# Optimization experiments

Hardware: AMD Instinct MI355X
Metric: run time of the kernel (lower is better)

The kernel has to match this reference:

```python
import jax, jax.numpy as jnp
import numpy as np

HEADS = 12
D_HEAD = 64  # d_model // heads


def _split_heads(t, heads, d_head):
    # Faithful to the torch code: transpose(1,2) -> (B, C, T), then
    # reshape (B, -1, heads, d_head), then transpose(1,2) -> (B, heads, T', d_head).
    B = t.shape[0]
    t = jnp.swapaxes(t, 1, 2)                      # (B, C, T)
    t = t.reshape(B, -1, heads, d_head)            # (B, T', heads, d_head) -- layout quirk preserved
    return jnp.swapaxes(t, 1, 2)                   # (B, heads, T', d_head)


def setup_inputs() -> dict:
    key = jax.random.key(0)
    ks = jax.random.split(key, 10)
    B, Tq, Tkv, D = 8, 4096, 77, 768
    s = 0.02
    return {
        "x": jax.random.normal(ks[0], (B, Tq, D), jnp.float32),
        "prompt": jax.random.normal(ks[1], (B, Tkv, D), jnp.float32),
        "Wq": jax.random.normal(ks[2], (D, D), jnp.float32) * s,
        "bq": jax.random.normal(ks[3], (D,), jnp.float32) * s,
        "Wk": jax.random.normal(ks[4], (D, D), jnp.float32) * s,
        "bk": jax.random.normal(ks[5], (D,), jnp.float32) * s,
        "Wv": jax.random.normal(ks[6], (D, D), jnp.float32) * s,
        "bv": jax.random.normal(ks[7], (D,), jnp.float32) * s,
        "Wp": jax.random.normal(ks[8], (D, D), jnp.float32) * s,
        "bp": jax.random.normal(ks[9], (D,), jnp.float32) * s,
    }


def reference(x, prompt, Wq, bq, Wk, bk, Wv, bv, Wp, bp):
    B, Tq, C = x.shape
    Ckv = prompt.shape[-1]
    q = _split_heads(x @ Wq.T + bq, HEADS, D_HEAD)       # (B, H, Tq, d_head)
    k = _split_heads(prompt @ Wk.T + bk, HEADS, D_HEAD)  # (B, H, Tkv, d_head)
    v = _split_heads(prompt @ Wv.T + bv, HEADS, D_HEAD)
    scale = 1.0 / jnp.sqrt(jnp.asarray(Ckv, x.dtype))    # note: sqrt(d_prompt), as in source
    att = jnp.einsum('bhqd,bhkd->bhqk', q, k) * scale
    att = jax.nn.softmax(att, axis=-1)
    out = jnp.einsum('bhqk,bhkd->bhqd', att, v)          # (B, H, Tq, d_head)
    out = jnp.swapaxes(out, 1, 2).reshape(B, Tq, C)
    return out @ Wp.T + bp                               # dropout = identity (eval)
```

## Files before the change

### kernel.cpp

```cpp
#include <hip/hip_runtime.h>

typedef __attribute__((ext_vector_type(8))) __bf16 bf16x8;
typedef __attribute__((ext_vector_type(4))) float f32x4;
typedef __attribute__((ext_vector_type(8))) unsigned short u16x8;
typedef __attribute__((ext_vector_type(4))) unsigned short u16x4;

#define DEV __device__ __forceinline__

DEV float bf2f(unsigned short u) {
  unsigned int x = ((unsigned int)u) << 16;
  return __builtin_bit_cast(float, x);
}
DEV unsigned short f2bf(float f) {
  unsigned int u = __builtin_bit_cast(unsigned int, f);
  u = u + 0x7fffu + ((u >> 16) & 1u);
  return (unsigned short)(u >> 16);
}

DEV void glds16(const void* g, void* l) {
  __builtin_amdgcn_global_load_lds(
      (__attribute__((address_space(1))) void*)g,
      (__attribute__((address_space(3))) void*)l, 16, 0, 0);
}

__global__ __launch_bounds__(256) void k_prep(
    const float* __restrict__ x, const float* __restrict__ Wq,
    const float* __restrict__ Wk, const float* __restrict__ Wv,
    const float* __restrict__ Wp, const float* __restrict__ prompt,
    const float* __restrict__ bk, const float* __restrict__ bv,
    unsigned short* __restrict__ xb, unsigned short* __restrict__ wqb,
    unsigned short* __restrict__ wkvb, unsigned short* __restrict__ wpb,
    unsigned short* __restrict__ pb, float* __restrict__ bkv,
    unsigned short* __restrict__ vt2) {
  const int blk = blockIdx.x;
  const int tid = threadIdx.x;
  if (blk < 2048) {
    for (int i = blk * 256 + tid; i < 6291456; i += 524288) {
      float4 v = reinterpret_cast<const float4*>(x)[i];
      u16x4 o;
      o[0] = f2bf(v.x); o[1] = f2bf(v.y); o[2] = f2bf(v.z); o[3] = f2bf(v.w);
      reinterpret_cast<u16x4*>(xb)[i] = o;
    }
  } else if (blk < 4352) {
    const int w = (blk - 2048) / 576;
    const int i = (blk - 2048 - w * 576) * 256 + tid;
    const float* src = (w == 0) ? Wq : (w == 1) ? Wk : (w == 2) ? Wv : Wp;
    unsigned short* dst =
        (w == 0) ? wqb : (w == 1) ? wkvb : (w == 2) ? (wkvb + 589824) : wpb;
    float4 v = reinterpret_cast<const float4*>(src)[i];
    u16x4 o;
    o[0] = f2bf(v.x); o[1] = f2bf(v.y); o[2] = f2bf(v.z); o[3] = f2bf(v.w);
    reinterpret_cast<u16x4*>(dst)[i] = o;
  } else if (blk < 5120) {
    const int i4 = (blk - 4352) * 256 + tid;
    const int e = i4 * 4;
    const int b = e / 98304;
    const int rem = e - b * 98304;
    const int s = rem / 768;
    const int d = rem - s * 768;
    u16x4 o;
    if (s < 77) {
      float4 v = *reinterpret_cast<const float4*>(&prompt[((long)b * 77 + s) * 768 + d]);
      o[0] = f2bf(v.x); o[1] = f2bf(v.y); o[2] = f2bf(v.z); o[3] = f2bf(v.w);
    } else {
      o[0] = 0; o[1] = 0; o[2] = 0; o[3] = 0;
    }
    reinterpret_cast<u16x4*>(pb)[i4] = o;
  } else if (blk < 5126) {
    const int i = (blk - 5120) * 256 + tid;
    if (i < 1536) bkv[i] = (i < 768) ? bk[i] : bv[i - 768];
  } else {
    const int i = (blk - 5126) * 256 + tid;
    u16x8 z = {};
    reinterpret_cast<u16x8*>(vt2)[i] = z;
  }
}

__global__ __launch_bounds__(256, 2) void k_gemmkv(const unsigned short* __restrict__ A,
                                                   const unsigned short* __restrict__ B, long sB,
                                                   unsigned short* __restrict__ Kv,
                                                   unsigned short* __restrict__ Vt2,
                                                   const float* __restrict__ bias) {
  __shared__ alignas(16) unsigned short As[128 * 64];
  __shared__ alignas(16) unsigned short Bs[128 * 64];

  const int bz = blockIdx.z;
  const unsigned short* Bb = B + (long)bz * sB;

  const int tid = threadIdx.x;
  const int wave = tid >> 6;
  const int lane = tid & 63;
  const int tm = blockIdx.y * 128;
  const int wm = (wave >> 1) * 64;
  const int wn = (wave & 1) * 64;
  const int fr = lane & 15;
  const int fk = (lane >> 4) * 8;
  const int srow = lane >> 3;
  const int scol = (lane & 7) * 8;

  f32x4 acc[4][4] = {};

  for (int k0 = 0; k0 < 768; k0 += 64) {
    __syncthreads();
#pragma unroll
    for (int i = 0; i < 4; ++i) {
      const int chunk = i * 4 + wave;
      glds16(A + (long)(tm + chunk * 8 + srow) * 768 + (k0 + scol), &As[chunk * 512]);
    }
#pragma unroll
    for (int i = 0; i < 4; ++i) {
      const int chunk = i * 4 + wave;
      glds16(Bb + (long)(chunk * 8 + srow) * 768 + (k0 + scol), &Bs[chunk * 512]);
    }
    __syncthreads();
#pragma unroll
    for (int ks = 0; ks < 2; ++ks) {
      bf16x8 af[4], bf[4];
#pragma unroll
      for (int mi = 0; mi < 4; ++mi)
        af[mi] = *reinterpret_cast<const bf16x8*>(&As[(wm + mi * 16 + fr) * 64 + ks * 32 + fk]);
#pragma unroll
      for (int ni = 0; ni < 4; ++ni)
        bf[ni] = *reinterpret_cast<const bf16x8*>(&Bs[(wn + ni * 16 + fr) * 64 + ks * 32 + fk]);
#pragma unroll
      for (int mi = 0; mi < 4; ++mi)
#pragma unroll
        for (int ni = 0; ni < 4; ++ni)
          acc[mi][ni] =
              __builtin_amdgcn_mfma_f32_16x16x32_bf16(af[mi], bf[ni], acc[mi][ni], 0, 0, 0);
    }
  }

  const int r0 = (lane >> 4) * 4;
#pragma unroll
  for (int mi = 0; mi < 4; ++mi) {
#pragma unroll
    for (int ni = 0; ni < 4; ++ni) {
      const int col = wn + ni * 16 + fr;
      if (col < 77) {
#pragma unroll
        for (int r = 0; r < 4; ++r) {
          const int row = tm + wm + mi * 16 + r0 + r;
          const unsigned short v = f2bf(acc[mi][ni][r] + bias[row]);
          if (tm < 768) {
            Kv[(long)bz * 59136 + (long)row * 77 + col] = v;
          } else {
            const int p = (row - 768) * 77 + col;
            const int snew = p / 768;
            const int c0 = p - snew * 768;
            Vt2[(long)bz * 79872 + (long)c0 * 104 + snew] = v;
          }
        }
      }
    }
  }
}

template <int QUIRK>
__global__ __launch_bounds__(256, 2) void k_g128(const unsigned short* __restrict__ A,
                                                 const unsigned short* __restrict__ B,
                                                 void* __restrict__ Cv,
                                                 const float* __restrict__ bias) {
  __shared__ alignas(16) unsigned short S[17408];
  unsigned short* const As = S;
  unsigned short* const Bs = S + 8192;

  const int tid = threadIdx.x;
  const int wave = tid >> 6;
  const int lane = tid & 63;
  const int l = (blockIdx.x & 7) * 192 + (blockIdx.x >> 3);
  const int tm = (QUIRK ? (l % 6) : (l / 6)) * 128;
  const int tn = (QUIRK ? (l / 6) : (l % 6)) * 128;
  const int wm = (wave >> 1) * 64;
  const int wn = (wave & 1) * 64;
  const int fr = lane & 15;
  const int fk = (lane >> 4) * 8;
  const int srow = lane >> 3;
  const int srcx = ((lane & 7) ^ srow) * 8;
  const int rx = (fr & 7) * 8;

  f32x4 acc[4][4] = {};

  for (int k0 = 0; k0 < 768; k0 += 64) {
    __syncthreads();
#pragma unroll
    for (int i = 0; i < 4; ++i) {
      const int chunk = i * 4 + wave;
      glds16(A + (long)(tm + chunk * 8 + srow) * 768 + (k0 + srcx), &As[chunk * 512]);
    }
#pragma unroll
    for (int i = 0; i < 4; ++i) {
      const int chunk = i * 4 + wave;
      glds16(B + (long)(tn + chunk * 8 + srow) * 768 + (k0 + srcx), &Bs[chunk * 512]);
    }
    __syncthreads();
#pragma unroll
    for (int ks = 0; ks < 2; ++ks) {
      bf16x8 af[4], bf[4];
#pragma unroll
      for (int mi = 0; mi < 4; ++mi)
        af[mi] = *reinterpret_cast<const bf16x8*>(
            &As[(wm + mi * 16 + fr) * 64 + ((ks * 32 + fk) ^ rx)]);
#pragma unroll
      for (int ni = 0; ni < 4; ++ni)
        bf[ni] = *reinterpret_cast<const bf16x8*>(
            &Bs[(wn + ni * 16 + fr) * 64 + ((ks * 32 + fk) ^ rx)]);
#pragma unroll
      for (int mi = 0; mi < 4; ++mi)
#pragma unroll
        for (int ni = 0; ni < 4; ++ni)
          acc[mi][ni] =
              __builtin_amdgcn_mfma_f32_16x16x32_bf16(af[mi], bf[ni], acc[mi][ni], 0, 0, 0);
    }
  }

  const int r0 = (lane >> 4) * 4;

  if (QUIRK) {
    __syncthreads();
#pragma unroll
    for (int mi = 0; mi < 4; ++mi)
#pragma unroll
      for (int ni = 0; ni < 4; ++ni)
#pragma unroll
        for (int r = 0; r < 4; ++r) {
          const int cm = wm + mi * 16 + r0 + r;
          const int ct = wn + ni * 16 + fr;
          S[cm * 136 + ct] = f2bf(acc[mi][ni][r] + bias[tm + cm]);
        }
    __syncthreads();
    unsigned short* qt = (unsigned short*)Cv;
    const int b_ = tn >> 12;
    const int toff = tn & 4095;
    const int cm = tid >> 1;
    const int t8 = (tid & 1) * 64;
    const long gb = (long)b_ * 3145728 + (long)(tm + cm) * 4096 + toff + t8;
#pragma unroll
    for (int j = 0; j < 8; ++j)
      *reinterpret_cast<u16x8*>(&qt[gb + j * 8]) =
          *reinterpret_cast<const u16x8*>(&S[cm * 136 + t8 + j * 8]);
  } else {
    float* out = (float*)Cv;
#pragma unroll
    for (int mi = 0; mi < 4; ++mi) {
#pragma unroll
      for (int ni = 0; ni < 4; ++ni) {
        const int col = tn + wn + ni * 16 + fr;
        const float bv = bias[col];
#pragma unroll
        for (int r = 0; r < 4; ++r) {
          const long g = tm + wm + mi * 16 + r0 + r;
          out[g * 768 + col] = acc[mi][ni][r] + bv;
        }
      }
    }
  }
}

__global__ __launch_bounds__(256, 4) void k_attn(const unsigned short* __restrict__ QT,
                                                 const unsigned short* __restrict__ KVT,
                                                 const unsigned short* __restrict__ VT2,
                                                 unsigned short* __restrict__ Y) {
  __shared__ alignas(16) unsigned short Plds[128 * 104];
  __shared__ alignas(16) unsigned short Vt[64 * 104];

  const int b = blockIdx.z;
  const int h = blockIdx.y;
  const int tid = threadIdx.x;
  const int wave = tid >> 6;
  const int lane = tid & 63;
  const int fr = lane & 15;
  const int fg = lane >> 4;

  const unsigned short* vsrc = VT2 + (long)b * 79872 + h * 6656;
#pragma unroll
  for (int r = 0; r < 4; ++r) {
    const int chunk = r * 256 + tid;
    if (chunk < 832) glds16(vsrc + chunk * 8, &Vt[chunk * 8]);
  }

  {
    const int row = wave * 32 + (lane >> 1);
    u16x8 z = {};
    *reinterpret_cast<u16x8*>(&Plds[row * 104 + 80 + (lane & 1) * 8]) = z;
  }

  const int t0 = blockIdx.x * 128 + wave * 32;
  const long qb = (long)b * 3145728 + h * 64;
  const long kflat = (long)b * 59136 + h * 64;

  bf16x8 qa[2][2];
#pragma unroll
  for (int m = 0; m < 2; ++m)
#pragma unroll
    for (int ks = 0; ks < 2; ++ks)
      qa[m][ks] = *reinterpret_cast<const bf16x8*>(
          &QT[qb + (long)(t0 + m * 16 + fr) * 768 + ks * 32 + fg * 8]);

  bf16x8 kb[5][2];
#pragma unroll
  for (int n = 0; n < 5; ++n)
#pragma unroll
    for (int ks = 0; ks < 2; ++ks)
      kb[n][ks] = *reinterpret_cast<const bf16x8*>(
          &KVT[kflat + (long)(n * 16 + fr) * 768 + ks * 32 + fg * 8]);

  f32x4 s_[2][5] = {};
#pragma unroll
  for (int ks = 0; ks < 2; ++ks)
#pragma unroll
    for (int m = 0; m < 2; ++m)
#pragma unroll
      for (int n = 0; n < 5; ++n)
        s_[m][n] = __builtin_amdgcn_mfma_f32_16x16x32_bf16(qa[m][ks], kb[n][ks], s_[m][n], 0, 0, 0);

  const float scale = 0.036084391824351615f;
  f32x4 rl[2];
#pragma unroll
  for (int m = 0; m < 2; ++m) {
#pragma unroll
    for (int n = 0; n < 5; ++n) {
      const int key = n * 16 + fr;
#pragma unroll
      for (int r = 0; r < 4; ++r)
        s_[m][n][r] = (key < 77) ? __expf(s_[m][n][r] * scale) : 0.f;
    }
    f32x4 t = s_[m][0] + s_[m][1] + s_[m][2] + s_[m][3] + s_[m][4];
#pragma unroll
    for (int w = 1; w < 16; w <<= 1) {
      f32x4 u;
#pragma unroll
      for (int r = 0; r < 4; ++r) u[r] = __shfl_xor(t[r], w);
      t += u;
    }
    rl[m][0] = 1.f / t[0]; rl[m][1] = 1.f / t[1];
    rl[m][2] = 1.f / t[2]; rl[m][3] = 1.f / t[3];
  }

#pragma unroll
  for (int m = 0; m < 2; ++m)
#pragma unroll
    for (int n = 0; n < 5; ++n)
#pragma unroll
      for (int r = 0; r < 4; ++r)
        Plds[(wave * 32 + m * 16 + fg * 4 + r) * 104 + n * 16 + fr] = f2bf(s_[m][n][r]);

  __syncthreads();

  f32x4 o[2][4] = {};
#pragma unroll
  for (int ks = 0; ks < 3; ++ks) {
    bf16x8 pa[2], vb[4];
#pragma unroll
    for (int m = 0; m < 2; ++m)
      pa[m] = *reinterpret_cast<const bf16x8*>(
          &Plds[(wave * 32 + m * 16 + fr) * 104 + ks * 32 + fg * 8]);
#pragma unroll
    for (int n = 0; n < 4; ++n)
      vb[n] = *reinterpret_cast<const bf16x8*>(&Vt[(n * 16 + fr) * 104 + ks * 32 + fg * 8]);
#pragma unroll
    for (int m = 0; m < 2; ++m)
#pragma unroll
      for (int n = 0; n < 4; ++n)
        o[m][n] = __builtin_amdgcn_mfma_f32_16x16x32_bf16(pa[m], vb[n], o[m][n], 0, 0, 0);
  }

#pragma unroll
  for (int m = 0; m < 2; ++m)
#pragma unroll
    for (int n = 0; n < 4; ++n)
#pragma unroll
      for (int r = 0; r < 4; ++r) {
        const int t = t0 + m * 16 + fg * 4 + r;
        const int d = n * 16 + fr;
        Y[qb + (long)t * 768 + d] = f2bf(o[m][n][r] * rl[m][r]);
      }
}

extern "C" void kernel_launch(void* const* d_in, const int* in_sizes, int n_in,
                              void* d_out, int out_size, void* d_ws, size_t ws_size,
                              hipStream_t stream) {
  const float* x      = (const float*)d_in[0];
  const float* prompt = (const float*)d_in[1];
  const float* Wq     = (const float*)d_in[2];
  const float* bq     = (const float*)d_in[3];
  const float* Wk     = (const float*)d_in[4];
  const float* bk     = (const float*)d_in[5];
  const float* Wv     = (const float*)d_in[6];
  const float* bv     = (const float*)d_in[7];
  const float* Wp     = (const float*)d_in[8];
  const float* bp     = (const float*)d_in[9];
  float* out = (float*)d_out;

  if (ws_size < 109185024u) return;
  char* ws = (char*)d_ws;
  unsigned short* xb   = (unsigned short*)(ws + 0);
  unsigned short* y    = xb;
  unsigned short* qt   = (unsigned short*)(ws + 50331648L);
  unsigned short* wqb  = (unsigned short*)(ws + 100663296L);
  unsigned short* wpb  = (unsigned short*)(ws + 101842944L);
  unsigned short* wkvb = (unsigned short*)(ws + 103022592L);
  unsigned short* pb   = (unsigned short*)(ws + 105381888L);
  unsigned short* kvt  = (unsigned short*)(ws + 106954752L);
  unsigned short* vt2  = (unsigned short*)(ws + 107900928L);
  float*          bkv  = (float*)(ws + 109178880L);

  k_prep<<<5438, 256, 0, stream>>>(x, Wq, Wk, Wv, Wp, prompt, bk, bv,
                                   xb, wqb, wkvb, wpb, pb, bkv, vt2);

  k_gemmkv<<<dim3(1, 12, 8), 256, 0, stream>>>(wkvb, pb, 98304L, kvt, vt2, bkv);

  k_g128<1><<<1536, 256, 0, stream>>>(wqb, xb, qt, bq);

  k_attn<<<dim3(32, 12, 8), 256, 0, stream>>>(qt, kvt, vt2, y);

  k_g128<0><<<1536, 256, 0, stream>>>(y, wpb, out, bp);
}
```

Measured before the change: 193.0 us.

## Merge KV and Q projection launches; pack bf16 converts and stage attention output

Folds the small K/V projection GEMM into the Q projection kernel as 96 extra blocks, removing one launch and letting the tiny KV work overlap with the Q GEMM. Replaces the scalar bf16 rounding with the packed v_cvt_pk_bf16_f32 instruction in the epilogues. The attention output is now staged through LDS and written as 16-byte vector stores instead of scattered 2-byte stores. The merged kernel adds a branch and uneven block costs, and the packed convert may round slightly differently from the manual routine.

```diff
diff --git a/kernel.cpp b/kernel.cpp
--- a/kernel.cpp
+++ b/kernel.cpp
@@ -15,6 +15,11 @@
   unsigned int u = __builtin_bit_cast(unsigned int, f);
   u = u + 0x7fffu + ((u >> 16) & 1u);
   return (unsigned short)(u >> 16);
+}
+DEV unsigned int cvtpk(float a, float b) {
+  unsigned int r;
+  asm("v_cvt_pk_bf16_f32 %0, %1, %2" : "=v"(r) : "v"(a), "v"(b));
+  return r;
 }
 
 DEV void glds16(const void* g, void* l) {
@@ -76,41 +81,107 @@
   }
 }
 
-__global__ __launch_bounds__(256, 2) void k_gemmkv(const unsigned short* __restrict__ A,
-                                                   const unsigned short* __restrict__ B, long sB,
-                                                   unsigned short* __restrict__ Kv,
-                                                   unsigned short* __restrict__ Vt2,
-                                                   const float* __restrict__ bias) {
-  __shared__ alignas(16) unsigned short As[128 * 64];
-  __shared__ alignas(16) unsigned short Bs[128 * 64];
-
-  const int bz = blockIdx.z;
-  const unsigned short* Bb = B + (long)bz * sB;
+__global__ __launch_bounds__(256, 2) void k_qkv(
+    const unsigned short* __restrict__ WQ, const unsigned short* __restrict__ XB,
+    unsigned short* __restrict__ QT, const float* __restrict__ BQ,
+    const unsigned short* __restrict__ WKV, const unsigned short* __restrict__ PB,
+    unsigned short* __restrict__ KV, unsigned short* __restrict__ VT2,
+    const float* __restrict__ BKV) {
+  __shared__ alignas(16) unsigned short S[17408];
+  unsigned short* const As = S;
+  unsigned short* const Bs = S + 8192;
 
   const int tid = threadIdx.x;
   const int wave = tid >> 6;
   const int lane = tid & 63;
-  const int tm = blockIdx.y * 128;
   const int wm = (wave >> 1) * 64;
   const int wn = (wave & 1) * 64;
   const int fr = lane & 15;
   const int fk = (lane >> 4) * 8;
   const int srow = lane >> 3;
-  const int scol = (lane & 7) * 8;
+  const int r0 = (lane >> 4) * 4;
+
+  if (blockIdx.x >= 1536) {
+    const int idx = blockIdx.x - 1536;
+    const int bz = idx / 12;
+    const int tm = (idx - bz * 12) * 128;
+    const unsigned short* Bb = PB + (long)bz * 98304;
+    const int scol = (lane & 7) * 8;
+
+    f32x4 acc[4][4] = {};
+    for (int k0 = 0; k0 < 768; k0 += 64) {
+      __syncthreads();
+#pragma unroll
+      for (int i = 0; i < 4; ++i) {
+        const int chunk = i * 4 + wave;
+        glds16(WKV + (long)(tm + chunk * 8 + srow) * 768 + (k0 + scol), &As[chunk * 512]);
+      }
+#pragma unroll
+      for (int i = 0; i < 4; ++i) {
+        const int chunk = i * 4 + wave;
+        glds16(Bb + (long)(chunk * 8 + srow) * 768 + (k0 + scol), &Bs[chunk * 512]);
+      }
+      __syncthreads();
+#pragma unroll
+      for (int ks = 0; ks < 2; ++ks) {
+        bf16x8 af[4], bf[4];
+#pragma unroll
+        for (int mi = 0; mi < 4; ++mi)
+          af[mi] = *reinterpret_cast<const bf16x8*>(&As[(wm + mi * 16 + fr) * 64 + ks * 32 + fk]);
+#pragma unroll
+        for (int ni = 0; ni < 4; ++ni)
+          bf[ni] = *reinterpret_cast<const bf16x8*>(&Bs[(wn + ni * 16 + fr) * 64 + ks * 32 + fk]);
+#pragma unroll
+        for (int mi = 0; mi < 4; ++mi)
+#pragma unroll
+          for (int ni = 0; ni < 4; ++ni)
+            acc[mi][ni] =
+                __builtin_amdgcn_mfma_f32_16x16x32_bf16(af[mi], bf[ni], acc[mi][ni], 0, 0, 0);
+      }
+    }
+#pragma unroll
+    for (int mi = 0; mi < 4; ++mi) {
+#pragma unroll
+      for (int ni = 0; ni < 4; ++ni) {
+        const int col = wn + ni * 16 + fr;
+        if (col < 77) {
+#pragma unroll
+          for (int r = 0; r < 4; ++r) {
+            const int row = tm + wm + mi * 16 + r0 + r;
+            const unsigned short v = f2bf(acc[mi][ni][r] + BKV[row]);
+            if (tm < 768) {
+              KV[(long)bz * 59136 + (long)row * 77 + col] = v;
+            } else {
+              const int p = (row - 768) * 77 + col;
+              const int snew = p / 768;
+              const int c0 = p - snew * 768;
+              VT2[(long)bz * 79872 + (long)c0 * 104 + snew] = v;
+            }
+          }
+        }
+      }
+    }
+    return;
+  }
+
+  const int l = (blockIdx.x & 7) * 192 + (blockIdx.x >> 3);
+  const int tm = (l % 6) * 128;
+  const int tn = (l / 6) * 128;
+  const int srcx = ((lane & 7) ^ srow) * 8;
+  const int rx = (fr & 7) * 8;
 
   f32x4 acc[4][4] = {};
-
   for (int k0 = 0; k0 < 768; k0 += 64) {
     __syncthreads();
 #pragma unroll
     for (int i = 0; i < 4; ++i) {
       const int chunk = i * 4 + wave;
-      glds16(A + (long)(tm + chunk * 8 + srow) * 768 + (k0 + scol), &As[chunk * 512]);
+      glds16(WQ + (long)(tm + chunk * 8 + srow) * 768 + (k0 + srcx), &As[chunk * 512]);
     }
 #pragma unroll
     for (int i = 0; i < 4; ++i) {
       const int chunk = i * 4 + wave;
-      glds16(Bb + (long)(chunk * 8 + srow) * 768 + (k0 + scol), &Bs[chunk * 512]);
+      glds16(XB + (long)(tn + chunk * 8 + srow) * 768 + (k0 + srcx), &Bs[chunk * 512]);
     }
     __syncthreads();
 #pragma unroll
@@ -118,10 +189,12 @@
       bf16x8 af[4], bf[4];
 #pragma unroll
       for (int mi = 0; mi < 4; ++mi)
-        af[mi] = *reinterpret_cast<const bf16x8*>(&As[(wm + mi * 16 + fr) * 64 + ks * 32 + fk]);
+        af[mi] = *reinterpret_cast<const bf16x8*>(
+            &As[(wm + mi * 16 + fr) * 64 + ((ks * 32 + fk) ^ rx)]);
 #pragma unroll
       for (int ni = 0; ni < 4; ++ni)
-        bf[ni] = *reinterpret_cast<const bf16x8*>(&Bs[(wn + ni * 16 + fr) * 64 + ks * 32 + fk]);
+        bf[ni] = *reinterpret_cast<const bf16x8*>(
+            &Bs[(wn + ni * 16 + fr) * 64 + ((ks * 32 + fk) ^ rx)]);
 #pragma unroll
       for (int mi = 0; mi < 4; ++mi)
 #pragma unroll
@@ -131,37 +204,40 @@
     }
   }
 
-  const int r0 = (lane >> 4) * 4;
+  __syncthreads();
 #pragma unroll
   for (int mi = 0; mi < 4; ++mi) {
+    const int cmb = wm + mi * 16 + r0;
 #pragma unroll
     for (int ni = 0; ni < 4; ++ni) {
-      const int col = wn + ni * 16 + fr;
-      if (col < 77) {
-#pragma unroll
-        for (int r = 0; r < 4; ++r) {
-          const int row = tm + wm + mi * 16 + r0 + r;
-          const unsigned short v = f2bf(acc[mi][ni][r] + bias[row]);
-          if (tm < 768) {
-            Kv[(long)bz * 59136 + (long)row * 77 + col] = v;
-          } else {
-            const int p = (row - 768) * 77 + col;
-            const int snew = p / 768;
-            const int c0 = p - snew * 768;
-            Vt2[(long)bz * 79872 + (long)c0 * 104 + snew] = v;
-          }
-        }
-      }
-    }
-  }
-}
-
-template <int QUIRK>
-__global__ __launch_bounds__(256, 2) void k_g128(const unsigned short* __restrict__ A,
+      const int ct = wn + ni * 16 + fr;
+      const unsigned int p01 =
+          cvtpk(acc[mi][ni][0] + BQ[tm + cmb], acc[mi][ni][1] + BQ[tm + cmb + 1]);
+      const unsigned int p23 =
+          cvtpk(acc[mi][ni][2] + BQ[tm + cmb + 2], acc[mi][ni][3] + BQ[tm + cmb + 3]);
+      S[(cmb + 0) * 136 + ct] = (unsigned short)p01;
+      S[(cmb + 1) * 136 + ct] = (unsigned short)(p01 >> 16);
+      S[(cmb + 2) * 136 + ct] = (unsigned short)p23;
+      S[(cmb + 3) * 136 + ct] = (unsigned short)(p23 >> 16);
+    }
+  }
+  __syncthreads();
+  const int b_ = tn >> 12;
+  const int toff = tn & 4095;
+  const int cm = tid >> 1;
+  const int t8 = (tid & 1) * 64;
+  const long gb = (long)b_ * 3145728 + (long)(tm + cm) * 4096 + toff + t8;
+#pragma unroll
+  for (int j = 0; j < 8; ++j)
+    *reinterpret_cast<u16x8*>(&QT[gb + j * 8]) =
+        *reinterpret_cast<const u16x8*>(&S[cm * 136 + t8 + j * 8]);
+}
+
+__global__ __launch_bounds__(256, 2) void k_gout(const unsigned short* __restrict__ A,
                                                  const unsigned short* __restrict__ B,
-                                                 void* __restrict__ Cv,
+                                                 float* __restrict__ out,
                                                  const float* __restrict__ bias) {
-  __shared__ alignas(16) unsigned short S[17408];
+  __shared__ alignas(16) unsigned short S[16384];
   unsigned short* const As = S;
   unsigned short* const Bs = S + 8192;
 
@@ -169,8 +245,8 @@
   const int wave = tid >> 6;
   const int lane = tid & 63;
   const int l = (blockIdx.x & 7) * 192 + (blockIdx.x >> 3);
-  const int tm = (QUIRK ? (l % 6) : (l / 6)) * 128;
-  const int tn = (QUIRK ? (l / 6) : (l % 6)) * 128;
+  const int tm = (l / 6) * 128;
+  const int tn = (l % 6) * 128;
   const int wm = (wave >> 1) * 64;
   const int wn = (wave & 1) * 64;
   const int fr = lane & 15;
@@ -215,43 +291,16 @@
   }
 
   const int r0 = (lane >> 4) * 4;
-
-  if (QUIRK) {
-    __syncthreads();
-#pragma unroll
-    for (int mi = 0; mi < 4; ++mi)
-#pragma unroll
-      for (int ni = 0; ni < 4; ++ni)
-#pragma unroll
-        for (int r = 0; r < 4; ++r) {
-          const int cm = wm + mi * 16 + r0 + r;
-          const int ct = wn + ni * 16 + fr;
-          S[cm * 136 + ct] = f2bf(acc[mi][ni][r] + bias[tm + cm]);
-        }
-    __syncthreads();
-    unsigned short* qt = (unsigned short*)Cv;
-    const int b_ = tn >> 12;
-    const int toff = tn & 4095;
-    const int cm = tid >> 1;
-    const int t8 = (tid & 1) * 64;
-    const long gb = (long)b_ * 3145728 + (long)(tm + cm) * 4096 + toff + t8;
-#pragma unroll
-    for (int j = 0; j < 8; ++j)
-      *reinterpret_cast<u16x8*>(&qt[gb + j * 8]) =
-          *reinterpret_cast<const u16x8*>(&S[cm * 136 + t8 + j * 8]);
-  } else {
-    float* out = (float*)Cv;
-#pragma unroll
-    for (int mi = 0; mi < 4; ++mi) {
-#pragma unroll
-      for (int ni = 0; ni < 4; ++ni) {
-        const int col = tn + wn + ni * 16 + fr;
-        const float bv = bias[col];
-#pragma unroll
-        for (int r = 0; r < 4; ++r) {
-          const long g = tm + wm + mi * 16 + r0 + r;
-          out[g * 768 + col] = acc[mi][ni][r] + bv;
-        }
+#pragma unroll
+  for (int mi = 0; mi < 4; ++mi) {
+#pragma unroll
+    for (int ni = 0; ni < 4; ++ni) {
+      const int col = tn + wn + ni * 16 + fr;
+      const float bv = bias[col];
+#pragma unroll
+      for (int r = 0; r < 4; ++r) {
+        const long g = tm + wm + mi * 16 + r0 + r;
+        out[g * 768 + col] = acc[mi][ni][r] + bv;
       }
     }
   }
@@ -340,10 +389,16 @@
 #pragma unroll
   for (int m = 0; m < 2; ++m)
 #pragma unroll
-    for (int n = 0; n < 5; ++n)
-#pragma unroll
-      for (int r = 0; r < 4; ++r)
-        Plds[(wave * 32 + m * 16 + fg * 4 + r) * 104 + n * 16 + fr] = f2bf(s_[m][n][r]);
+    for (int n = 0; n < 5; ++n) {
+      const unsigned int p01 = cvtpk(s_[m][n][0], s_[m][n][1]);
+      const unsigned int p23 = cvtpk(s_[m][n][2], s_[m][n][3]);
+      const int base = wave * 32 + m * 16 + fg * 4;
+      const int col = n * 16 + fr;
+      Plds[(base + 0) * 104 + col] = (unsigned short)p01;
+      Plds[(base + 1) * 104 + col] = (unsigned short)(p01 >> 16);
+      Plds[(base + 2) * 104 + col] = (unsigned short)p23;
+      Plds[(base + 3) * 104 + col] = (unsigned short)(p23 >> 16);
+    }
 
   __syncthreads();
 
@@ -368,13 +423,24 @@
 #pragma unroll
   for (int m = 0; m < 2; ++m)
 #pragma unroll
-    for (int n = 0; n < 4; ++n)
-#pragma unroll
-      for (int r = 0; r < 4; ++r) {
-        const int t = t0 + m * 16 + fg * 4 + r;
-        const int d = n * 16 + fr;
-        Y[qb + (long)t * 768 + d] = f2bf(o[m][n][r] * rl[m][r]);
-      }
+    for (int n = 0; n < 4; ++n) {
+      const unsigned int p01 = cvtpk(o[m][n][0] * rl[m][0], o[m][n][1] * rl[m][1]);
+      const unsigned int p23 = cvtpk(o[m][n][2] * rl[m][2], o[m][n][3] * rl[m][3]);
+      const int base = wave * 32 + m * 16 + fg * 4;
+      const int col = n * 16 + fr;
+      Plds[(base + 0) * 104 + col] = (unsigned short)p01;
+      Plds[(base + 1) * 104 + col] = (unsigned short)(p01 >> 16);
+      Plds[(base + 2) * 104 + col] = (unsigned short)p23;
+      Plds[(base + 3) * 104 + col] = (unsigned short)(p23 >> 16);
+    }
+#pragma unroll
+  for (int j = 0; j < 4; ++j) {
+    const int chunk = j * 64 + lane;
+    const int row = chunk >> 3;
+    const int d8 = (chunk & 7) * 8;
+    *reinterpret_cast<u16x8*>(&Y[qb + (long)(t0 + row) * 768 + d8]) =
+        *reinterpret_cast<const u16x8*>(&Plds[(wave * 32 + row) * 104 + d8]);
+  }
 }
 
 extern "C" void kernel_launch(void* const* d_in, const int* in_sizes, int n_in,
@@ -408,11 +474,9 @@
   k_prep<<<5438, 256, 0, stream>>>(x, Wq, Wk, Wv, Wp, prompt, bk, bv,
                                    xb, wqb, wkvb, wpb, pb, bkv, vt2);
 
-  k_gemmkv<<<dim3(1, 12, 8), 256, 0, stream>>>(wkvb, pb, 98304L, kvt, vt2, bkv);
-
-  k_g128<1><<<1536, 256, 0, stream>>>(wqb, xb, qt, bq);
+  k_qkv<<<1632, 256, 0, stream>>>(wqb, xb, qt, bq, wkvb, pb, kvt, vt2, bkv);
 
   k_attn<<<dim3(32, 12, 8), 256, 0, stream>>>(qt, kvt, vt2, y);
 
-  k_g128<0><<<1536, 256, 0, stream>>>(y, wpb, out, bp);
-}
+  k_gout<<<1536, 256, 0, stream>>>(y, wpb, out, bp);
+}
```

New measurement: 181.7 us. -5.9%, faster.
